# Optimization experiments

Hardware: AMD Instinct MI355X
Metric: run time of the kernel (lower is better)

Reference implementation:

```python
import jax, jax.numpy as jnp
import numpy as np

ALPHA = 0.2          # LeakyReLU negative slope
NEG_FILL = -9e15     # mask value used by the original module


def setup_inputs() -> dict:
    key = jax.random.key(0)
    k1, k2, k3, k4 = jax.random.split(key, 4)
    N, D, H, F = 4096, 512, 8, 64  # nhid*nheads == embedding_dim
    h = jax.random.normal(k1, (N, D), dtype=jnp.float32)
    adj = jax.random.randint(k2, (N, N), 0, 2, dtype=jnp.int32)
    # per-head linear projection weights (no bias) and attention vectors
    W = jax.random.normal(k3, (H, D, F), dtype=jnp.float32) * (1.0 / np.sqrt(D))
    a = jax.random.normal(k4, (H, 2 * F), dtype=jnp.float32) * 0.1
    return {"h": h, "adj": adj, "W": W, "a": a}


def reference(h, adj, W, a):
    H, D, F = W.shape
    N = h.shape[0]
    # per-head projection: [H, N, F]
    hp = jnp.einsum('nd,hdf->hnf', h, W)
    # score(i,j) = leakyrelu(a[:F].h_i + a[F:].h_j)  (decomposed broadcast-add,
    # same math as the original N*N concat construction)
    a_src, a_dst = a[:, :F], a[:, F:]
    f_src = jnp.einsum('hnf,hf->hn', hp, a_src)  # [H, N]
    f_dst = jnp.einsum('hnf,hf->hn', hp, a_dst)  # [H, N]
    e = jax.nn.leaky_relu(f_src[:, :, None] + f_dst[:, None, :], ALPHA)  # [H,N,N]
    e = jnp.where(adj[None] > 0, e, NEG_FILL)
    att = jax.nn.softmax(e, axis=-1)  # softmax over neighbors j (dim=1 in torch)
    out = jnp.einsum('hij,hjf->hif', att, hp)  # [H, N, F]
    # concat heads -> [N, H*F], then ELU
    out = jnp.transpose(out, (1, 0, 2)).reshape(N, H * F)
    return jax.nn.elu(out)
```

## Files before the change

kernel.cpp:

```cpp
#include <hip/hip_runtime.h>

#define NN 4096
#define DD 512
#define HH 8
#define FF 64
#define LRELU_ALPHA 0.2f
#define SP 72
#define JSPLIT 2
#define JCHUNK (NN / JSPLIT)

typedef __attribute__((ext_vector_type(8))) short bf16x8;
typedef __attribute__((ext_vector_type(4))) float f32x4;

__device__ __forceinline__ float f4c(const float4& v, int k) {
    return k == 0 ? v.x : (k == 1 ? v.y : (k == 2 ? v.z : v.w));
}
__device__ __forceinline__ void f4s(float4& v, int k, float x) {
    if (k == 0) v.x = x; else if (k == 1) v.y = x; else if (k == 2) v.z = x; else v.w = x;
}
__device__ __forceinline__ unsigned short f2bf(float x) {
    unsigned u = __float_as_uint(x);
    return (unsigned short)((u + 0x7fffu + ((u >> 16) & 1u)) >> 16);
}
__device__ __forceinline__ float bf2f(unsigned short h) {
    return __uint_as_float(((unsigned)h) << 16);
}
__device__ __forceinline__ unsigned fkey(float x) {
    unsigned u = __float_as_uint(x);
    return (u & 0x80000000u) ? ~u : (u | 0x80000000u);
}
__device__ __forceinline__ float funkey(unsigned k) {
    unsigned u = (k & 0x80000000u) ? (k ^ 0x80000000u) : ~k;
    return __uint_as_float(u);
}

__global__ __launch_bounds__(256) void k_prep(const int* __restrict__ adj,
                                              const float* __restrict__ W,
                                              unsigned long long* __restrict__ adjm,
                                              unsigned short* __restrict__ wt_hi,
                                              unsigned short* __restrict__ wt_lo,
                                              unsigned* __restrict__ mxkey,
                                              float* __restrict__ hpsum) {
    __shared__ unsigned long long shbuf[2080];
    int b = blockIdx.x, t = threadIdx.x;
    if (b < 1024) {
        int g = b >> 2, cq = b & 3;
        int r0 = g * 16;
        int lane = t & 63, wv = t >> 6;
        unsigned long long (*w64)[17] = (unsigned long long(*)[17])shbuf;
        for (int r = 0; r < 16; r++) {
            #pragma unroll
            for (int q = 0; q < 4; q++) {
                int col = cq * 1024 + q * 256 + t;
                unsigned long long m = __ballot(adj[(size_t)(r0 + r) * NN + col] > 0);
                if (lane == 0) w64[r][q * 4 + wv] = m;
            }
        }
        __syncthreads();
        for (int tt = wv; tt < 16; tt += 4) {
            unsigned long long wbits = w64[lane & 15][tt];
            unsigned long long my = 0;
            #pragma unroll
            for (int k = 0; k < 16; k++) {
                int shv = 32 * (k >> 3) + 8 * (lane >> 4) + (k & 7);
                unsigned long long bal = __ballot((unsigned)((wbits >> shv) & 1ULL));
                if (lane == k) my = bal;
            }
            if (lane < 16)
                adjm[((size_t)g * 64 + cq * 16 + tt) * 16 + lane] = my;
        }
    } else if (b < 1088) {
        float (*tile)[65] = (float(*)[65])shbuf;
        int idx = b - 1024;
        int h = idx >> 3;
        int d0 = (idx & 7) * 64;
        #pragma unroll
        for (int kidx = 0; kidx < 4; kidx++) {
            int id = t + 256 * kidx;
            int dd = id >> 4, f4i = (id & 15) * 4;
            float4 v = *(const float4*)(W + ((size_t)(h * DD + d0 + dd)) * FF + f4i);
            tile[dd][f4i] = v.x; tile[dd][f4i + 1] = v.y;
            tile[dd][f4i + 2] = v.z; tile[dd][f4i + 3] = v.w;
        }
        __syncthreads();
        int f = t >> 2, c = (t & 3) * 16;
        union { unsigned short s[16]; uint4 v[2]; } hb, lb;
        #pragma unroll
        for (int q = 0; q < 16; q++) {
            float v = tile[c + q][f];
            unsigned short hi = f2bf(v);
            hb.s[q] = hi;
            lb.s[q] = f2bf(v - bf2f(hi));
        }
        uint4* dh = (uint4*)(wt_hi + ((size_t)h * FF + f) * DD + d0 + c);
        uint4* dl = (uint4*)(wt_lo + ((size_t)h * FF + f) * DD + d0 + c);
        dh[0] = hb.v[0]; dh[1] = hb.v[1];
        dl[0] = lb.v[0]; dl[1] = lb.v[1];
    } else {
        if (t < 16) mxkey[t] = 0u;
        hpsum[t] = 0.f;
        hpsum[t + 256] = 0.f;
    }
}

__global__ __launch_bounds__(256) void k_hp_mfma(const float* __restrict__ hmat,
                                                 const unsigned short* __restrict__ whi,
                                                 const unsigned short* __restrict__ wlo,
                                                 const float* __restrict__ a,
                                                 unsigned short* __restrict__ hpT_hi,
                                                 float* __restrict__ fs,
                                                 float* __restrict__ fd,
                                                 float* __restrict__ hpsum,
                                                 unsigned* __restrict__ mxkey) {
    __shared__ char smem[4 * 64 * SP * 2];
    unsigned short* ah = (unsigned short*)smem;
    unsigned short* al = ah + 64 * SP;
    unsigned short* bh = al + 64 * SP;
    unsigned short* bl = bh + 64 * SP;

    int t = threadIdx.x;
    int h = blockIdx.y;
    int n0 = blockIdx.x * 64;
    int lane = t & 63;
    int w = t >> 6;
    int R0 = (w >> 1) * 32, F0 = (w & 1) * 32;
    int am = lane & 15, aq = lane >> 4;
    int sr = t >> 2, sc = (t & 3) * 16;

    const float* gha = hmat + (size_t)(n0 + sr) * DD;
    const unsigned short* gbh = whi + ((size_t)h * FF + sr) * DD;
    const unsigned short* gbl = wlo + ((size_t)h * FF + sr) * DD;

    f32x4 acc[2][2] = {};
    for (int kk = 0; kk < DD; kk += 64) {
        {
            float4 p0 = *(const float4*)(gha + kk + sc);
            float4 p1 = *(const float4*)(gha + kk + sc + 4);
            float4 p2 = *(const float4*)(gha + kk + sc + 8);
            float4 p3 = *(const float4*)(gha + kk + sc + 12);
            union { unsigned short s[16]; uint4 v[2]; } hb, lb;
            #pragma unroll
            for (int q = 0; q < 16; q++) {
                float v = q < 4 ? f4c(p0, q) : q < 8 ? f4c(p1, q - 4)
                          : q < 12 ? f4c(p2, q - 8) : f4c(p3, q - 12);
                unsigned short hi = f2bf(v);
                hb.s[q] = hi;
                lb.s[q] = f2bf(v - bf2f(hi));
            }
            *(uint4*)(ah + sr * SP + sc) = hb.v[0]; *(uint4*)(ah + sr * SP + sc + 8) = hb.v[1];
            *(uint4*)(al + sr * SP + sc) = lb.v[0]; *(uint4*)(al + sr * SP + sc + 8) = lb.v[1];
        }
        {
            const uint4* s2 = (const uint4*)(gbh + kk + sc);
            const uint4* s3 = (const uint4*)(gbl + kk + sc);
            uint4 w0 = s2[0], w1 = s2[1], x0 = s3[0], x1 = s3[1];
            *(uint4*)(bh + sr * SP + sc) = w0; *(uint4*)(bh + sr * SP + sc + 8) = w1;
            *(uint4*)(bl + sr * SP + sc) = x0; *(uint4*)(bl + sr * SP + sc + 8) = x1;
        }
        __syncthreads();
        #pragma unroll
        for (int k2 = 0; k2 < 2; k2++) {
            int ko = k2 * 32 + aq * 8;
            bf16x8 a0h = *(const bf16x8*)(ah + (R0 + am) * SP + ko);
            bf16x8 a1h = *(const bf16x8*)(ah + (R0 + 16 + am) * SP + ko);
            bf16x8 a0l = *(const bf16x8*)(al + (R0 + am) * SP + ko);
            bf16x8 a1l = *(const bf16x8*)(al + (R0 + 16 + am) * SP + ko);
            bf16x8 b0h = *(const bf16x8*)(bh + (F0 + am) * SP + ko);
            bf16x8 b1h = *(const bf16x8*)(bh + (F0 + 16 + am) * SP + ko);
            bf16x8 b0l = *(const bf16x8*)(bl + (F0 + am) * SP + ko);
            bf16x8 b1l = *(const bf16x8*)(bl + (F0 + 16 + am) * SP + ko);
            acc[0][0] = __builtin_amdgcn_mfma_f32_16x16x32_bf16(a0h, b0h, acc[0][0], 0, 0, 0);
            acc[0][1] = __builtin_amdgcn_mfma_f32_16x16x32_bf16(a0h, b1h, acc[0][1], 0, 0, 0);
            acc[1][0] = __builtin_amdgcn_mfma_f32_16x16x32_bf16(a1h, b0h, acc[1][0], 0, 0, 0);
            acc[1][1] = __builtin_amdgcn_mfma_f32_16x16x32_bf16(a1h, b1h, acc[1][1], 0, 0, 0);
            acc[0][0] = __builtin_amdgcn_mfma_f32_16x16x32_bf16(a0h, b0l, acc[0][0], 0, 0, 0);
            acc[0][1] = __builtin_amdgcn_mfma_f32_16x16x32_bf16(a0h, b1l, acc[0][1], 0, 0, 0);
            acc[1][0] = __builtin_amdgcn_mfma_f32_16x16x32_bf16(a1h, b0l, acc[1][0], 0, 0, 0);
            acc[1][1] = __builtin_amdgcn_mfma_f32_16x16x32_bf16(a1h, b1l, acc[1][1], 0, 0, 0);
            acc[0][0] = __builtin_amdgcn_mfma_f32_16x16x32_bf16(a0l, b0h, acc[0][0], 0, 0, 0);
            acc[0][1] = __builtin_amdgcn_mfma_f32_16x16x32_bf16(a0l, b1h, acc[0][1], 0, 0, 0);
            acc[1][0] = __builtin_amdgcn_mfma_f32_16x16x32_bf16(a1l, b0h, acc[1][0], 0, 0, 0);
            acc[1][1] = __builtin_amdgcn_mfma_f32_16x16x32_bf16(a1l, b1h, acc[1][1], 0, 0, 0);
        }
        __syncthreads();
    }

    unsigned* tt = (unsigned*)smem;
    float* rs = (float*)(smem + 17408);
    float* rd = rs + 256;
    float* ash = rd + 256;
    if (t < 128) ash[t] = a[h * 2 * FF + t];
    int col = lane & 15, rbase = (lane >> 4) * 4;
    #pragma unroll
    for (int m16 = 0; m16 < 2; m16++) {
        #pragma unroll
        for (int n16 = 0; n16 < 2; n16++) {
            #pragma unroll
            for (int r = 0; r < 4; r++) {
                int nl = R0 + m16 * 16 + rbase + r;
                int f = F0 + n16 * 16 + col;
                float v = acc[m16][n16][r];
                unsigned short hi = f2bf(v);
                unsigned short lo = f2bf(v - bf2f(hi));
                tt[f * 68 + nl] = (unsigned)hi | ((unsigned)lo << 16);
            }
        }
    }
    __syncthreads();
    {
        int f = t >> 2, c = (t & 3) * 16;
        union { unsigned short s[16]; uint4 v[2]; } hb;
        float csum = 0.f;
        #pragma unroll
        for (int q = 0; q < 16; q++) {
            unsigned u = tt[f * 68 + c + q];
            hb.s[q] = (unsigned short)(u & 0xffffu);
            csum += bf2f((unsigned short)(u & 0xffffu)) + bf2f((unsigned short)(u >> 16));
        }
        uint4* dh = (uint4*)(hpT_hi + ((size_t)h * FF + f) * NN + n0 + c);
        dh[0] = hb.v[0]; dh[1] = hb.v[1];
        csum += __shfl_xor(csum, 1);
        csum += __shfl_xor(csum, 2);
        if ((t & 3) == 0) unsafeAtomicAdd(hpsum + h * FF + f, csum);
    }
    {
        int n = t & 63, g = t >> 6;
        float fsp = 0.f, fdp = 0.f;
        #pragma unroll
        for (int q = 0; q < 16; q++) {
            int f = g * 16 + q;
            unsigned u = tt[f * 68 + n];
            float v = bf2f((unsigned short)(u & 0xffffu)) + bf2f((unsigned short)(u >> 16));
            fsp += v * ash[f];
            fdp += v * ash[64 + f];
        }
        rs[g * 64 + n] = fsp;
        rd[g * 64 + n] = fdp;
    }
    __syncthreads();
    if (t < 64) {
        const float LOG2E = 1.44269504f;
        float fdv = (rd[t] + rd[64 + t] + rd[128 + t] + rd[192 + t]) * LOG2E;
        fs[(size_t)h * NN + n0 + t] = (rs[t] + rs[64 + t] + rs[128 + t] + rs[192 + t]) * LOG2E;
        fd[(size_t)h * NN + n0 + t] = fdv;
        unsigned key = fkey(fdv);
        #pragma unroll
        for (int off = 32; off; off >>= 1) key = max(key, (unsigned)__shfl_xor((int)key, off));
        if (t == 0) atomicMax(mxkey + h, key);
    }
}

__global__ __launch_bounds__(512) void k_attn(const float* __restrict__ fs,
                                              const float* __restrict__ fd,
                                              const unsigned* __restrict__ mxkey,
                                              const unsigned long long* __restrict__ adjm,
                                              const unsigned short* __restrict__ hpT_hi,
                                              const float* __restrict__ hpsum,
                                              float* __restrict__ outp) {
    __shared__ unsigned short hbh[2][2][64 * SP];

    int t = threadIdx.x;
    int h = blockIdx.y;
    int i0 = blockIdx.x * 64;
    int lane = t & 63;
    int w = t >> 6;
    int h2 = w >> 2;
    int rg = w & 3;
    int am = lane & 15, aq = lane >> 4;
    int th = t >> 8;
    int ts = t & 255;
    int sr = ts >> 2, sc = (ts & 3) * 16;

    float mfdL = funkey(mxkey[h]);
    float fsv = fs[(size_t)h * NN + i0 + rg * 16 + am];
    float sL = fsv + mfdL;
    float mrL = fmaxf(sL, LRELU_ALPHA * sL);
    float Ai = fsv - mrL;
    float Ci = -0.8f * mrL;

    int rgu = __builtin_amdgcn_readfirstlane(rg);
    int h2u = __builtin_amdgcn_readfirstlane(h2);
    const unsigned long long* mbase = adjm + ((size_t)(blockIdx.x * 4 + rgu) * 64) * 16;
    const unsigned short* gH = hpT_hi + (size_t)h * FF * NN;
    const float* fdh = fd + (size_t)h * NN + (size_t)h2u * JCHUNK;

    f32x4 acc[4] = {};
    f32x4 accl = {};
    bf16x8 ones;
    #pragma unroll
    for (int i = 0; i < 8; i++) ones[i] = (short)0x3f80;

    auto stage_load = [&](int j0, uint4& v0, uint4& v1) {
        const uint4* s = (const uint4*)(gH + (size_t)sr * NN + th * JCHUNK + j0 + sc);
        v0 = s[0]; v1 = s[1];
    };
    auto stage_write = [&](int buf, uint4 v0, uint4 v1) {
        *(uint4*)(&hbh[buf][th][sr * SP + sc]) = v0;
        *(uint4*)(&hbh[buf][th][sr * SP + sc + 8]) = v1;
    };
    auto fd_load = [&](int j0, float4* p) {
        p[0] = *(const float4*)(fdh + j0 + aq * 8);
        p[1] = *(const float4*)(fdh + j0 + aq * 8 + 4);
        p[2] = *(const float4*)(fdh + j0 + 32 + aq * 8);
        p[3] = *(const float4*)(fdh + j0 + 32 + aq * 8 + 4);
    };
    auto mkfrag = [&](float4 p0, float4 p1, const unsigned long long* mk, int off) -> bf16x8 {
        unsigned eu[8];
        #pragma unroll
        for (int q = 0; q < 2; q++) {
            float4 pv = q ? p1 : p0;
            #pragma unroll
            for (int bq = 0; bq < 4; bq++) {
                float tv = Ai + f4c(pv, bq);
                float uv = __builtin_fmaf(LRELU_ALPHA, tv, Ci);
                float ev = __builtin_amdgcn_exp2f(fmaxf(tv, uv));
                unsigned r;
                asm("v_cndmask_b32 %0, 0, %1, %2"
                    : "=v"(r) : "v"(ev), "s"(mk[off + q * 4 + bq]));
                eu[q * 4 + bq] = r;
            }
        }
        union { unsigned u[4]; bf16x8 v; } pk;
        pk.u[0] = __builtin_amdgcn_perm(eu[1], eu[0], 0x07060302);
        pk.u[1] = __builtin_amdgcn_perm(eu[3], eu[2], 0x07060302);
        pk.u[2] = __builtin_amdgcn_perm(eu[5], eu[4], 0x07060302);
        pk.u[3] = __builtin_amdgcn_perm(eu[7], eu[6], 0x07060302);
        return pk.v;
    };

    bf16x8 Pc0, Pc1;
    {
        uint4 v0, v1; float4 pf[4];
        stage_load(0, v0, v1);
        fd_load(0, pf);
        unsigned long long mk[16];
        #pragma unroll
        for (int k = 0; k < 16; k++) mk[k] = mbase[(size_t)(h2u * 32) * 16 + k];
        Pc0 = mkfrag(pf[0], pf[1], mk, 0);
        Pc1 = mkfrag(pf[2], pf[3], mk, 8);
        stage_write(0, v0, v1);
        __syncthreads();
    }

    for (int j0 = 0; j0 < JCHUNK; j0 += 64) {
        int cur = (j0 >> 6) & 1;
        int jn = (j0 + 64) & (JCHUNK - 1);
        uint4 v0, v1; float4 pf[4];
        stage_load(jn, v0, v1);
        fd_load(jn, pf);
        unsigned long long mk[16];
        #pragma unroll
        for (int k = 0; k < 16; k++) mk[k] = mbase[(size_t)(h2u * 32 + (jn >> 6)) * 16 + k];

        #pragma unroll
        for (int k2 = 0; k2 < 2; k2++) {
            int ko = k2 * 32 + aq * 8;
            bf16x8 x0 = *(const bf16x8*)(&hbh[cur][h2][(am)      * SP + ko]);
            bf16x8 x1 = *(const bf16x8*)(&hbh[cur][h2][(am + 16) * SP + ko]);
            bf16x8 x2 = *(const bf16x8*)(&hbh[cur][h2][(am + 32) * SP + ko]);
            bf16x8 x3 = *(const bf16x8*)(&hbh[cur][h2][(am + 48) * SP + ko]);
            bf16x8 P = k2 ? Pc1 : Pc0;
            acc[0] = __builtin_amdgcn_mfma_f32_16x16x32_bf16(x0, P, acc[0], 0, 0, 0);
            acc[1] = __builtin_amdgcn_mfma_f32_16x16x32_bf16(x1, P, acc[1], 0, 0, 0);
            acc[2] = __builtin_amdgcn_mfma_f32_16x16x32_bf16(x2, P, acc[2], 0, 0, 0);
            acc[3] = __builtin_amdgcn_mfma_f32_16x16x32_bf16(x3, P, acc[3], 0, 0, 0);
            accl   = __builtin_amdgcn_mfma_f32_16x16x32_bf16(ones, P, accl, 0, 0, 0);
        }

        stage_write(cur ^ 1, v0, v1);
        Pc0 = mkfrag(pf[0], pf[1], mk, 0);
        Pc1 = mkfrag(pf[2], pf[3], mk, 8);
        __syncthreads();
    }

    float* cb = (float*)hbh;
    if (h2 == 1) {
        #pragma unroll
        for (int mf = 0; mf < 4; mf++)
            *(f32x4*)&cb[((rg * 4 + mf) * 64 + lane) * 4] = acc[mf];
        cb[4096 + rg * 64 + lane] = accl[0];
    }
    __syncthreads();
    if (h2 == 0) {
        #pragma unroll
        for (int mf = 0; mf < 4; mf++) {
            f32x4 o = *(const f32x4*)&cb[((rg * 4 + mf) * 64 + lane) * 4];
            acc[mf] += o;
        }
        float li = accl[0] + cb[4096 + rg * 64 + lane];
        const float invN = 1.0f / NN;
        float rl = 1.f / li;
        int row = i0 + rg * 16 + am;
        float* orow = outp + (size_t)row * (HH * FF) + h * FF;
        #pragma unroll
        for (int mf = 0; mf < 4; mf++) {
            float4 ov;
            #pragma unroll
            for (int r = 0; r < 4; r++) {
                int f = mf * 16 + aq * 4 + r;
                float v;
                if (li > 0.f) v = acc[mf][r] * rl;
                else          v = hpsum[h * FF + f] * invN;
                v = v > 0.f ? v : __expf(v) - 1.f;
                f4s(ov, r, v);
            }
            *(float4*)(orow + mf * 16 + aq * 4) = ov;
        }
    }
}

extern "C" void kernel_launch(void* const* d_in, const int* in_sizes, int n_in,
                              void* d_out, int out_size, void* d_ws, size_t ws_size,
                              hipStream_t stream) {
    const float* hmat = (const float*)d_in[0];
    const int*   adj  = (const int*)d_in[1];
    const float* W    = (const float*)d_in[2];
    const float* a    = (const float*)d_in[3];
    float* out = (float*)d_out;

    char* ws = (char*)d_ws;
    unsigned short* hpT_hi = (unsigned short*)(ws);
    unsigned long long* adjm = (unsigned long long*)(ws + (4u << 20));
    unsigned short* wt_hi  = (unsigned short*)(ws + (6u << 20));
    unsigned short* wt_lo  = (unsigned short*)(ws + (6u << 20) + (512u << 10));
    float* fs    = (float*)(ws + (7u << 20));
    float* fd    = (float*)(ws + (7u << 20) + (128u << 10));
    unsigned* mxkey = (unsigned*)(ws + (7u << 20) + (256u << 10));
    float* hpsum = (float*)(mxkey + 16);

    k_prep   <<<dim3(1089),          256, 0, stream>>>(adj, W, adjm, wt_hi, wt_lo,
                                                       mxkey, hpsum);
    k_hp_mfma<<<dim3(64, 8),         256, 0, stream>>>(hmat, wt_hi, wt_lo, a,
                                                       hpT_hi, fs, fd, hpsum, mxkey);
    k_attn   <<<dim3(NN / 64, HH),   512, 0, stream>>>(fs, fd, mxkey, adjm,
                                                       hpT_hi, hpsum, out);
}
```

Measured before the change: 186.6 us.

## Pre-split h into bf16 hi/lo once in prep kernel and widen adjacency packing grid

Moves the fp32-to-bf16 hi/lo split of the input features out of the projection GEMM, which previously redid it for each of the 8 heads, into new blocks of the prep kernel that write h_hi/h_lo to workspace. The GEMM now loads pre-split bf16 tiles directly. The adjacency bit-packing is also split across twice as many blocks, each handling 512 columns, to raise parallelism in the prep kernel. The cost is an extra 8 MB write-then-read round trip through workspace plus a larger prep launch.

```diff
diff --git a/kernel.cpp b/kernel.cpp
--- a/kernel.cpp
+++ b/kernel.cpp
@@ -36,29 +36,32 @@
 
 __global__ __launch_bounds__(256) void k_prep(const int* __restrict__ adj,
                                               const float* __restrict__ W,
+                                              const float* __restrict__ hmat,
                                               unsigned long long* __restrict__ adjm,
                                               unsigned short* __restrict__ wt_hi,
                                               unsigned short* __restrict__ wt_lo,
+                                              unsigned short* __restrict__ h_hi,
+                                              unsigned short* __restrict__ h_lo,
                                               unsigned* __restrict__ mxkey,
                                               float* __restrict__ hpsum) {
     __shared__ unsigned long long shbuf[2080];
     int b = blockIdx.x, t = threadIdx.x;
-    if (b < 1024) {
-        int g = b >> 2, cq = b & 3;
+    if (b < 2048) {
+        int g = b >> 3, cs = b & 7;
         int r0 = g * 16;
         int lane = t & 63, wv = t >> 6;
-        unsigned long long (*w64)[17] = (unsigned long long(*)[17])shbuf;
+        unsigned long long (*w64)[9] = (unsigned long long(*)[9])shbuf;
         for (int r = 0; r < 16; r++) {
             #pragma unroll
-            for (int q = 0; q < 4; q++) {
-                int col = cq * 1024 + q * 256 + t;
+            for (int q = 0; q < 2; q++) {
+                int col = cs * 512 + q * 256 + t;
                 unsigned long long m = __ballot(adj[(size_t)(r0 + r) * NN + col] > 0);
                 if (lane == 0) w64[r][q * 4 + wv] = m;
             }
         }
         __syncthreads();
-        for (int tt = wv; tt < 16; tt += 4) {
-            unsigned long long wbits = w64[lane & 15][tt];
+        for (int tl = wv; tl < 8; tl += 4) {
+            unsigned long long wbits = w64[lane & 15][tl];
             unsigned long long my = 0;
             #pragma unroll
             for (int k = 0; k < 16; k++) {
@@ -67,11 +70,11 @@
                 if (lane == k) my = bal;
             }
             if (lane < 16)
-                adjm[((size_t)g * 64 + cq * 16 + tt) * 16 + lane] = my;
-        }
-    } else if (b < 1088) {
+                adjm[((size_t)g * 64 + cs * 8 + tl) * 16 + lane] = my;
+        }
+    } else if (b < 2112) {
         float (*tile)[65] = (float(*)[65])shbuf;
-        int idx = b - 1024;
+        int idx = b - 2048;
         int h = idx >> 3;
         int d0 = (idx & 7) * 64;
         #pragma unroll
@@ -96,6 +99,31 @@
         uint4* dl = (uint4*)(wt_lo + ((size_t)h * FF + f) * DD + d0 + c);
         dh[0] = hb.v[0]; dh[1] = hb.v[1];
         dl[0] = lb.v[0]; dl[1] = lb.v[1];
+    } else if (b < 2368) {
+        int idx = b - 2112;
+        int row = idx * 16 + (t >> 4);
+        int c0 = (t & 15) * 32;
+        const float* src = hmat + (size_t)row * DD + c0;
+        #pragma unroll
+        for (int half = 0; half < 2; half++) {
+            float4 p0 = *(const float4*)(src + half * 16);
+            float4 p1 = *(const float4*)(src + half * 16 + 4);
+            float4 p2 = *(const float4*)(src + half * 16 + 8);
+            float4 p3 = *(const float4*)(src + half * 16 + 12);
+            union { unsigned short s[16]; uint4 v[2]; } hb, lb;
+            #pragma unroll
+            for (int q = 0; q < 16; q++) {
+                float v = q < 4 ? f4c(p0, q) : q < 8 ? f4c(p1, q - 4)
+                          : q < 12 ? f4c(p2, q - 8) : f4c(p3, q - 12);
+                unsigned short hi = f2bf(v);
+                hb.s[q] = hi;
+                lb.s[q] = f2bf(v - bf2f(hi));
+            }
+            uint4* dh = (uint4*)(h_hi + (size_t)row * DD + c0 + half * 16);
+            uint4* dl = (uint4*)(h_lo + (size_t)row * DD + c0 + half * 16);
+            dh[0] = hb.v[0]; dh[1] = hb.v[1];
+            dl[0] = lb.v[0]; dl[1] = lb.v[1];
+        }
     } else {
         if (t < 16) mxkey[t] = 0u;
         hpsum[t] = 0.f;
@@ -103,7 +131,8 @@
     }
 }
 
-__global__ __launch_bounds__(256) void k_hp_mfma(const float* __restrict__ hmat,
+__global__ __launch_bounds__(256) void k_hp_mfma(const unsigned short* __restrict__ hhi,
+                                                 const unsigned short* __restrict__ hlo,
                                                  const unsigned short* __restrict__ whi,
                                                  const unsigned short* __restrict__ wlo,
                                                  const float* __restrict__ a,
@@ -127,28 +156,19 @@
     int am = lane & 15, aq = lane >> 4;
     int sr = t >> 2, sc = (t & 3) * 16;
 
-    const float* gha = hmat + (size_t)(n0 + sr) * DD;
+    const unsigned short* ghh = hhi + (size_t)(n0 + sr) * DD;
+    const unsigned short* ghl = hlo + (size_t)(n0 + sr) * DD;
     const unsigned short* gbh = whi + ((size_t)h * FF + sr) * DD;
     const unsigned short* gbl = wlo + ((size_t)h * FF + sr) * DD;
 
     f32x4 acc[2][2] = {};
     for (int kk = 0; kk < DD; kk += 64) {
         {
-            float4 p0 = *(const float4*)(gha + kk + sc);
-            float4 p1 = *(const float4*)(gha + kk + sc + 4);
-            float4 p2 = *(const float4*)(gha + kk + sc + 8);
-            float4 p3 = *(const float4*)(gha + kk + sc + 12);
-            union { unsigned short s[16]; uint4 v[2]; } hb, lb;
-            #pragma unroll
-            for (int q = 0; q < 16; q++) {
-                float v = q < 4 ? f4c(p0, q) : q < 8 ? f4c(p1, q - 4)
-                          : q < 12 ? f4c(p2, q - 8) : f4c(p3, q - 12);
-                unsigned short hi = f2bf(v);
-                hb.s[q] = hi;
-                lb.s[q] = f2bf(v - bf2f(hi));
-            }
-            *(uint4*)(ah + sr * SP + sc) = hb.v[0]; *(uint4*)(ah + sr * SP + sc + 8) = hb.v[1];
-            *(uint4*)(al + sr * SP + sc) = lb.v[0]; *(uint4*)(al + sr * SP + sc + 8) = lb.v[1];
+            const uint4* s0 = (const uint4*)(ghh + kk + sc);
+            const uint4* s1 = (const uint4*)(ghl + kk + sc);
+            uint4 h0 = s0[0], h1 = s0[1], l0 = s1[0], l1 = s1[1];
+            *(uint4*)(ah + sr * SP + sc) = h0; *(uint4*)(ah + sr * SP + sc + 8) = h1;
+            *(uint4*)(al + sr * SP + sc) = l0; *(uint4*)(al + sr * SP + sc + 8) = l1;
         }
         {
             const uint4* s2 = (const uint4*)(gbh + kk + sc);
@@ -427,10 +447,12 @@
     float* fd    = (float*)(ws + (7u << 20) + (128u << 10));
     unsigned* mxkey = (unsigned*)(ws + (7u << 20) + (256u << 10));
     float* hpsum = (float*)(mxkey + 16);
-
-    k_prep   <<<dim3(1089),          256, 0, stream>>>(adj, W, adjm, wt_hi, wt_lo,
-                                                       mxkey, hpsum);
-    k_hp_mfma<<<dim3(64, 8),         256, 0, stream>>>(hmat, wt_hi, wt_lo, a,
+    unsigned short* h_hi = (unsigned short*)(ws + (8u << 20));
+    unsigned short* h_lo = (unsigned short*)(ws + (12u << 20));
+
+    k_prep   <<<dim3(2369),          256, 0, stream>>>(adj, W, hmat, adjm, wt_hi, wt_lo,
+                                                       h_hi, h_lo, mxkey, hpsum);
+    k_hp_mfma<<<dim3(64, 8),         256, 0, stream>>>(h_hi, h_lo, wt_hi, wt_lo, a,
                                                        hpT_hi, fs, fd, hpsum, mxkey);
     k_attn   <<<dim3(NN / 64, HH),   512, 0, stream>>>(fs, fd, mxkey, adjm,
                                                        hpT_hi, hpsum, out);
```

Result: faster. 175.2 us (median of 2 runs) (-6.1%).
